# Kernel optimization log

Hardware: AMD Instinct MI355X
Metric: run time of the kernel (lower is better)

Reference implementation:

```python
import jax, jax.numpy as jnp
import numpy as np
import math

HIDDEN = 1024
N_HEADS = 16
HEAD_DIM = HIDDEN // N_HEADS  # 64
B, S = 4, 8192


def setup_inputs() -> dict:
    key = jax.random.key(0)
    ks = jax.random.split(key, 5)
    scale = 1.0 / math.sqrt(HIDDEN)
    return {
        "hidden_states": jax.random.normal(ks[0], (B, S, HIDDEN), dtype=jnp.float32),
        "Wq": jax.random.normal(ks[1], (HIDDEN, HIDDEN), dtype=jnp.float32) * scale,
        "Wk": jax.random.normal(ks[2], (HIDDEN, HIDDEN), dtype=jnp.float32) * scale,
        "Wv": jax.random.normal(ks[3], (HIDDEN, HIDDEN), dtype=jnp.float32) * scale,
        "Wo": jax.random.normal(ks[4], (HIDDEN, HIDDEN), dtype=jnp.float32) * scale,
    }


def reference(hidden_states, Wq, Wk, Wv, Wo):
    b, s, _ = hidden_states.shape
    # nn.Linear(bias=False): y = x @ W.T
    q = (hidden_states @ Wq.T).reshape(b, s, N_HEADS, HEAD_DIM)
    k = (hidden_states @ Wk.T).reshape(b, s, N_HEADS, HEAD_DIM)
    v = (hidden_states @ Wv.T).reshape(b, s, N_HEADS, HEAD_DIM)
    # Faithful to source: NO transpose to (b,h,s,d); matmul contracts head_dim
    # per (batch, position), yielding [b, s, h, h] head-mixing weights.
    attn = jnp.einsum("bshd,bstd->bsht", q, k) / math.sqrt(HEAD_DIM)
    attn = jax.nn.softmax(attn, axis=-1)
    out = jnp.einsum("bsht,bstd->bshd", attn, v).reshape(b, s, HIDDEN)
    return out @ Wo.T
```

## Files before the change

kernel.cpp:

```cpp
#include <hip/hip_runtime.h>
#include <hip/hip_bf16.h>


typedef short bf16x8 __attribute__((ext_vector_type(8)));
typedef float f32x4  __attribute__((ext_vector_type(4)));

__device__ __forceinline__ float bf2f(short u) {
    union { unsigned int ui; float f; } cv;
    cv.ui = ((unsigned int)(unsigned short)u) << 16;
    return cv.f;
}
__device__ __forceinline__ short f2bf(float f) {
    __hip_bfloat16 h = __float2bfloat16(f);
    return *reinterpret_cast<short*>(&h);
}

__device__ __forceinline__ void gload_lds16(const void* g, void* lds) {
    const unsigned __attribute__((address_space(1)))* gp =
        reinterpret_cast<const unsigned __attribute__((address_space(1)))*>((unsigned long long)g);
    unsigned __attribute__((address_space(3)))* lp =
        reinterpret_cast<unsigned __attribute__((address_space(3)))*>(
            (unsigned int)(unsigned long long)lds);
    __builtin_amdgcn_global_load_lds(gp, lp, 16, 0, 0);
}

__global__ void detect_dtype(const unsigned* __restrict__ x, int* __restrict__ flag) {
    __shared__ int cnt;
    if (threadIdx.x == 0) cnt = 0;
    __syncthreads();
    int c = 0;
    for (int i = threadIdx.x; i < 4096; i += 256) {
        const unsigned u = x[(long)i * 4001 + 3];
        const unsigned b = (u >> 7) & 0xFF;
        c += (b >= 0x70 && b <= 0x87) ? 1 : 0;
    }
    atomicAdd(&cnt, c);
    __syncthreads();
    if (threadIdx.x == 0) *flag = (cnt > 2048) ? 0 : 1;
}

__global__ void convert_any(const void* __restrict__ src, long eoff,
                            short* __restrict__ dst, long n,
                            const int* __restrict__ flag) {
    const int f = *flag;
    const long step = (long)gridDim.x * blockDim.x * 8;
    for (long i = ((long)blockIdx.x * blockDim.x + threadIdx.x) * 8; i < n; i += step) {
        if (f) {
            const float* s = (const float*)src + eoff + i;
            const f32x4 a = *(const f32x4*)s;
            const f32x4 b = *(const f32x4*)(s + 4);
            bf16x8 o;
            o[0] = f2bf(a[0]); o[1] = f2bf(a[1]); o[2] = f2bf(a[2]); o[3] = f2bf(a[3]);
            o[4] = f2bf(b[0]); o[5] = f2bf(b[1]); o[6] = f2bf(b[2]); o[7] = f2bf(b[3]);
            *(bf16x8*)(dst + i) = o;
        } else {
            *(bf16x8*)(dst + i) = *(const bf16x8*)((const short*)src + eoff + i);
        }
    }
}

__device__ __forceinline__ void gemm256_core(const short* __restrict__ A,
                                             const short* __restrict__ W,
                                             void* __restrict__ C,
                                             const int* flag_fp32,
                                             long m0, int n0, short* lds) {
    constexpr int K = 1024, N = 1024;
    const int tid  = threadIdx.x;
    const int lane = tid & 63;
    const int wid  = tid >> 6;
    const int wm = wid >> 2, wn = wid & 3;

    short* A0 = lds;
    short* B0 = lds + 16384;
    short* A1 = lds + 32768;
    short* B1 = lds + 49152;

    const int srl = tid >> 3;
    const int kcs = (tid & 7) ^ (srl & 7);
    int aoff[4], boff[4];
    #pragma unroll
    for (int i = 0; i < 4; ++i) {
        const int row = i * 64 + srl;
        aoff[i] = (int)((m0 + row) * K + kcs * 8);
        boff[i] = (n0 + row) * K + kcs * 8;
    }
    const int ldsw = wid * 512;

    f32x4 acc[8][4] = {};

    #pragma unroll
    for (int i = 0; i < 4; ++i) gload_lds16(A + aoff[i], A0 + i * 4096 + ldsw);
    #pragma unroll
    for (int i = 0; i < 4; ++i) gload_lds16(W + boff[i], B0 + i * 4096 + ldsw);

    for (int t = 0; t < 16; ++t) {
        const int cur = t & 1;
        const short* rA = cur ? A1 : A0;
        const short* rB = cur ? B1 : B0;
        short* sA = cur ? A0 : A1;
        short* sB = cur ? B0 : B1;
        const int kadd = (t + 1) * 64;
        const bool more = (t < 15);

        #pragma unroll
        for (int q = 0; q < 4; ++q) {
            if (more) {
                if (q == 0) {
                    gload_lds16(A + aoff[0] + kadd, sA + 0 * 4096 + ldsw);
                    gload_lds16(A + aoff[1] + kadd, sA + 1 * 4096 + ldsw);
                } else if (q == 1) {
                    gload_lds16(A + aoff[2] + kadd, sA + 2 * 4096 + ldsw);
                    gload_lds16(A + aoff[3] + kadd, sA + 3 * 4096 + ldsw);
                } else if (q == 2) {
                    gload_lds16(W + boff[0] + kadd, sB + 0 * 4096 + ldsw);
                    gload_lds16(W + boff[1] + kadd, sB + 1 * 4096 + ldsw);
                } else {
                    gload_lds16(W + boff[2] + kadd, sB + 2 * 4096 + ldsw);
                    gload_lds16(W + boff[3] + kadd, sB + 3 * 4096 + ldsw);
                }
            }
            if (q == 0) {
                if (more) asm volatile("s_waitcnt vmcnt(2)" ::: "memory");
                else      asm volatile("s_waitcnt vmcnt(0)" ::: "memory");
            }
            __builtin_amdgcn_s_barrier();
            __builtin_amdgcn_sched_barrier(0);
            const int mfh = q >> 1, ks = q & 1;
            const int kx8 = ((ks * 4 + (lane >> 4)) ^ (lane & 7)) * 8;
            bf16x8 af[4], bfr[4];
            #pragma unroll
            for (int m = 0; m < 4; ++m)
                af[m] = *(const bf16x8*)(rA + (wm * 128 + (mfh * 4 + m) * 16 + (lane & 15)) * 64 + kx8);
            #pragma unroll
            for (int n = 0; n < 4; ++n)
                bfr[n] = *(const bf16x8*)(rB + (wn * 64 + n * 16 + (lane & 15)) * 64 + kx8);
            __builtin_amdgcn_s_setprio(1);
            #pragma unroll
            for (int m = 0; m < 4; ++m)
                #pragma unroll
                for (int n = 0; n < 4; ++n)
                    acc[mfh * 4 + m][n] = __builtin_amdgcn_mfma_f32_16x16x32_bf16(
                                              af[m], bfr[n], acc[mfh * 4 + m][n], 0, 0, 0);
            __builtin_amdgcn_s_setprio(0);
            __builtin_amdgcn_s_barrier();
        }
    }

    const int f = flag_fp32 ? *flag_fp32 : 0;
    #pragma unroll
    for (int mf = 0; mf < 8; ++mf) {
        #pragma unroll
        for (int nf = 0; nf < 4; ++nf) {
            const int  col   = n0 + wn * 64 + nf * 16 + (lane & 15);
            const long rbase = m0 + wm * 128 + mf * 16 + (lane >> 4) * 4;
            if (f) {
                float* Cf = (float*)C;
                #pragma unroll
                for (int r = 0; r < 4; ++r)
                    Cf[(rbase + r) * N + col] = acc[mf][nf][r];
            } else {
                short* Cs = (short*)C;
                #pragma unroll
                for (int r = 0; r < 4; ++r)
                    Cs[(rbase + r) * N + col] = f2bf(acc[mf][nf][r]);
            }
        }
    }
}

__global__ __launch_bounds__(512, 2) void gemm_qkv256(const short* __restrict__ A,
                                                      const short* __restrict__ W0,
                                                      const short* __restrict__ W1,
                                                      const short* __restrict__ W2,
                                                      short* __restrict__ C0,
                                                      short* __restrict__ C1,
                                                      short* __restrict__ C2) {
    __shared__ __align__(16) short lds[65536];
    const int nwg = gridDim.x;
    const int q8  = nwg >> 3;
    const int d   = blockIdx.x;
    const int lin = (d & 7) * q8 + (d >> 3);
    const int x   = lin / 12;
    const int r   = lin - x * 12;
    const int yy  = r / 3;
    const int z   = r - yy * 3;
    const short* W = (z == 0) ? W0 : (z == 1) ? W1 : W2;
    short*       C = (z == 0) ? C0 : (z == 1) ? C1 : C2;
    gemm256_core(A, W, C, nullptr, (long)x * 256, yy * 256, lds);
}

__global__ __launch_bounds__(512, 2) void gemm_out256(const short* __restrict__ A,
                                                      const short* __restrict__ W,
                                                      void* __restrict__ C,
                                                      long moff,
                                                      const int* __restrict__ flag) {
    __shared__ __align__(16) short lds[65536];
    const int nwg = gridDim.x;
    const int q8  = nwg >> 3;
    const int d   = blockIdx.x;
    const int lin = (d & 7) * q8 + (d >> 3);
    const int x   = lin >> 2;
    const int yy  = lin & 3;
    gemm256_core(A, W, C, flag, moff + (long)x * 256, yy * 256, lds);
}

__global__ __launch_bounds__(256) void attn_mix(const short* __restrict__ Q,
                                                const short* __restrict__ K,
                                                const short* __restrict__ V,
                                                short* __restrict__ Z) {
    constexpr int RS = 72;
    __shared__ short sq[4][16 * RS];
    __shared__ short sk[4][16 * RS];
    __shared__ short sv[4][16 * RS];
    __shared__ float sp[4][256];

    const int  tid  = threadIdx.x;
    const int  lane = tid & 63;
    const int  w    = tid >> 6;
    const long tok  = (long)blockIdx.x * 4 + w;

    const short* qg = Q + tok * 1024;
    const short* kg = K + tok * 1024;
    const short* vg = V + tok * 1024;

    #pragma unroll
    for (int it = 0; it < 2; ++it) {
        const int c   = lane + 64 * it;
        const int row = c >> 3;
        const int cc  = (c & 7) * 8;
        *(bf16x8*)&sq[w][row * RS + cc] = *(const bf16x8*)(qg + c * 8);
        *(bf16x8*)&sk[w][row * RS + cc] = *(const bf16x8*)(kg + c * 8);
        *(bf16x8*)&sv[w][row * RS + cc] = *(const bf16x8*)(vg + c * 8);
    }
    __syncthreads();

    const int h  = lane >> 2;
    const int t0 = (lane & 3) * 4;
    float sc[4] = {0.f, 0.f, 0.f, 0.f};
    for (int d = 0; d < 64; ++d) {
        const float qv = bf2f(sq[w][h * RS + d]);
        #pragma unroll
        for (int j = 0; j < 4; ++j)
            sc[j] += qv * bf2f(sk[w][(t0 + j) * RS + d]);
    }
    #pragma unroll
    for (int j = 0; j < 4; ++j) sc[j] *= 0.125f;

    float mx = fmaxf(fmaxf(sc[0], sc[1]), fmaxf(sc[2], sc[3]));
    mx = fmaxf(mx, __shfl_xor(mx, 1));
    mx = fmaxf(mx, __shfl_xor(mx, 2));
    float ex[4], s = 0.f;
    #pragma unroll
    for (int j = 0; j < 4; ++j) { ex[j] = __expf(sc[j] - mx); s += ex[j]; }
    s += __shfl_xor(s, 1);
    s += __shfl_xor(s, 2);
    const float inv = 1.f / s;
    #pragma unroll
    for (int j = 0; j < 4; ++j) sp[w][h * 16 + t0 + j] = ex[j] * inv;
    __syncthreads();

    const int dbase = (lane & 3) * 16;
    float o[16] = {};
    for (int t = 0; t < 16; ++t) {
        const float p = sp[w][h * 16 + t];
        const bf16x8 v0 = *(const bf16x8*)&sv[w][t * RS + dbase];
        const bf16x8 v1 = *(const bf16x8*)&sv[w][t * RS + dbase + 8];
        #pragma unroll
        for (int e = 0; e < 8; ++e) {
            o[e]     += p * bf2f(v0[e]);
            o[e + 8] += p * bf2f(v1[e]);
        }
    }
    bf16x8 ov0, ov1;
    #pragma unroll
    for (int e = 0; e < 8; ++e) { ov0[e] = f2bf(o[e]); ov1[e] = f2bf(o[e + 8]); }
    *(bf16x8*)(Z + tok * 1024 + lane * 16)     = ov0;
    *(bf16x8*)(Z + tok * 1024 + lane * 16 + 8) = ov1;
}

extern "C" void kernel_launch(void* const* d_in, const int* in_sizes, int n_in,
                              void* d_out, int out_size, void* d_ws, size_t ws_size,
                              hipStream_t stream) {
    const void* X = d_in[0];

    const long TOT = 32768;
    constexpr long WELEM = 1024 * 1024;

    char* ws   = (char*)d_ws;
    int*  flag = (int*)ws;
    short* Wqb = (short*)(ws + 256);
    short* Wkb = Wqb + WELEM;
    short* Wvb = Wkb + WELEM;
    short* Wob = Wvb + WELEM;
    short* dyn = Wob + WELEM;

    const size_t fixed = 256 + 4 * WELEM * 2;
    long chunk = 256;
    const long tiers[4] = {32768, 8192, 2048, 512};
    for (int i = 0; i < 4; ++i)
        if (fixed + (size_t)6 * tiers[i] * 1024 * 2 <= ws_size) { chunk = tiers[i]; break; }

    short* Xb = dyn;
    short* Qb = Xb + chunk * 1024;
    short* Kb = Qb + chunk * 1024;
    short* Vb = Kb + chunk * 1024;
    short* Zb = Vb + chunk * 1024;

    detect_dtype<<<1, 256, 0, stream>>>((const unsigned*)X, flag);
    convert_any<<<512, 256, 0, stream>>>(d_in[1], 0, Wqb, WELEM, flag);
    convert_any<<<512, 256, 0, stream>>>(d_in[2], 0, Wkb, WELEM, flag);
    convert_any<<<512, 256, 0, stream>>>(d_in[3], 0, Wvb, WELEM, flag);
    convert_any<<<512, 256, 0, stream>>>(d_in[4], 0, Wob, WELEM, flag);

    for (long t0 = 0; t0 < TOT; t0 += chunk) {
        convert_any<<<2048, 256, 0, stream>>>(X, t0 * 1024, Xb, chunk * 1024, flag);
        gemm_qkv256<<<dim3((chunk / 256) * 12), 512, 0, stream>>>(Xb, Wqb, Wkb, Wvb,
                                                                  Qb, Kb, Vb);
        attn_mix<<<dim3(chunk / 4), 256, 0, stream>>>(Qb, Kb, Vb, Zb);
        gemm_out256<<<dim3((chunk / 256) * 4), 512, 0, stream>>>(Zb - t0 * 1024, Wob,
                                                                 d_out, t0, flag);
    }
}
```

Baseline: 415.5 us.

## Restructure GEMM main loop into two k-substeps with fewer barriers

Reorganizes the inner loop of the LDS double-buffered bf16 GEMM from four quarter-steps into two k-substeps that each load all 8 A fragments and 4 B fragments before issuing 32 MFMAs. Prefetch of the next tile moves to after the fragment reads and a barrier, A in the first substep and B in the second, and the vmcnt wait drops from every step to the end of each tile. The aim is fewer barriers and waits per tile and longer MFMA bursts. In exchange it holds more fragment registers and waits fully on each tile's global loads at the end of the iteration, which may expose memory latency.

```diff
diff --git a/kernel.cpp b/kernel.cpp
--- a/kernel.cpp
+++ b/kernel.cpp
@@ -92,6 +92,8 @@
     for (int i = 0; i < 4; ++i) gload_lds16(A + aoff[i], A0 + i * 4096 + ldsw);
     #pragma unroll
     for (int i = 0; i < 4; ++i) gload_lds16(W + boff[i], B0 + i * 4096 + ldsw);
+    asm volatile("s_waitcnt vmcnt(0)" ::: "memory");
+    __builtin_amdgcn_s_barrier();
 
     for (int t = 0; t < 16; ++t) {
         const int cur = t & 1;
@@ -103,46 +105,44 @@
         const bool more = (t < 15);
 
         #pragma unroll
-        for (int q = 0; q < 4; ++q) {
-            if (more) {
-                if (q == 0) {
-                    gload_lds16(A + aoff[0] + kadd, sA + 0 * 4096 + ldsw);
-                    gload_lds16(A + aoff[1] + kadd, sA + 1 * 4096 + ldsw);
-                } else if (q == 1) {
-                    gload_lds16(A + aoff[2] + kadd, sA + 2 * 4096 + ldsw);
-                    gload_lds16(A + aoff[3] + kadd, sA + 3 * 4096 + ldsw);
-                } else if (q == 2) {
-                    gload_lds16(W + boff[0] + kadd, sB + 0 * 4096 + ldsw);
-                    gload_lds16(W + boff[1] + kadd, sB + 1 * 4096 + ldsw);
-                } else {
-                    gload_lds16(W + boff[2] + kadd, sB + 2 * 4096 + ldsw);
-                    gload_lds16(W + boff[3] + kadd, sB + 3 * 4096 + ldsw);
-                }
-            }
-            if (q == 0) {
-                if (more) asm volatile("s_waitcnt vmcnt(2)" ::: "memory");
-                else      asm volatile("s_waitcnt vmcnt(0)" ::: "memory");
-            }
-            __builtin_amdgcn_s_barrier();
-            __builtin_amdgcn_sched_barrier(0);
-            const int mfh = q >> 1, ks = q & 1;
+        for (int ks = 0; ks < 2; ++ks) {
             const int kx8 = ((ks * 4 + (lane >> 4)) ^ (lane & 7)) * 8;
-            bf16x8 af[4], bfr[4];
+            bf16x8 af[8], bfr[4];
             #pragma unroll
-            for (int m = 0; m < 4; ++m)
-                af[m] = *(const bf16x8*)(rA + (wm * 128 + (mfh * 4 + m) * 16 + (lane & 15)) * 64 + kx8);
+            for (int m = 0; m < 8; ++m)
+                af[m] = *(const bf16x8*)(rA + (wm * 128 + m * 16 + (lane & 15)) * 64 + kx8);
             #pragma unroll
             for (int n = 0; n < 4; ++n)
                 bfr[n] = *(const bf16x8*)(rB + (wn * 64 + n * 16 + (lane & 15)) * 64 + kx8);
+            __builtin_amdgcn_sched_barrier(0);
+            __builtin_amdgcn_s_barrier();
+            __builtin_amdgcn_sched_barrier(0);
+            if (more) {
+                if (ks == 0) {
+                    #pragma unroll
+                    for (int i = 0; i < 4; ++i)
+                        gload_lds16(A + aoff[i] + kadd, sA + i * 4096 + ldsw);
+                } else {
+                    #pragma unroll
+                    for (int i = 0; i < 4; ++i)
+                        gload_lds16(W + boff[i] + kadd, sB + i * 4096 + ldsw);
+                }
+            }
+            asm volatile("s_waitcnt lgkmcnt(0)" ::: "memory");
+            __builtin_amdgcn_sched_barrier(0);
             __builtin_amdgcn_s_setprio(1);
             #pragma unroll
-            for (int m = 0; m < 4; ++m)
+            for (int m = 0; m < 8; ++m)
                 #pragma unroll
                 for (int n = 0; n < 4; ++n)
-                    acc[mfh * 4 + m][n] = __builtin_amdgcn_mfma_f32_16x16x32_bf16(
-                                              af[m], bfr[n], acc[mfh * 4 + m][n], 0, 0, 0);
+                    acc[m][n] = __builtin_amdgcn_mfma_f32_16x16x32_bf16(
+                                    af[m], bfr[n], acc[m][n], 0, 0, 0);
             __builtin_amdgcn_s_setprio(0);
-            __builtin_amdgcn_s_barrier();
+            __builtin_amdgcn_sched_barrier(0);
+            if (ks == 1) {
+                asm volatile("s_waitcnt vmcnt(0)" ::: "memory");
+                __builtin_amdgcn_s_barrier();
+            }
         }
     }
 
```

Measured after the change: 415.5 us. About the same (-0.0%).
